# Optimization experiments

Measured on AMD Instinct MI355X. Metric: run time of the kernel, lower is better.

The kernel has to match this reference:

```python
import jax, jax.numpy as jnp
import numpy as np

B, S, D, H = 8, 1024, 1024, 16
DH = D // H
LN_EPS = 1e-5
SLOPE = 0.01  # nn.LeakyReLU default negative_slope


def _ln(x, g, b):
    m = x.mean(-1, keepdims=True)
    v = ((x - m) ** 2).mean(-1, keepdims=True)
    return (x - m) / jnp.sqrt(v + LN_EPS) * g + b


def _leaky(x):
    return jnp.where(x >= 0, x, SLOPE * x)


def setup_inputs() -> dict:
    key = jax.random.key(0)
    ks = jax.random.split(key, 6)
    q = jax.random.normal(ks[0], (B, S, D), dtype=jnp.float32)
    masks = jnp.ones((B, S), dtype=jnp.int32)  # all-valid mask (masked_fill is a no-op)
    w1 = jax.random.normal(ks[1], (D, D), dtype=jnp.float32) * 0.02
    b1 = jnp.zeros((D,), jnp.float32)
    w2 = jax.random.normal(ks[2], (D, D), dtype=jnp.float32) * 0.02
    b2 = jnp.zeros((D,), jnp.float32)
    ones = jnp.ones((D,), jnp.float32)
    zeros = jnp.zeros((D,), jnp.float32)
    return dict(q=q, masks=masks,
                w1=w1, b1=b1, ln1_g=ones, ln1_b=zeros,
                w2=w2, b2=b2, ln2_g=ones, ln2_b=zeros,
                anf_g=ones, anf_b=zeros,
                an1_g=ones, an1_b=zeros,
                an2_g=ones, an2_b=zeros)


def reference(q, masks, w1, b1, ln1_g, ln1_b, w2, b2, ln2_g, ln2_b,
              anf_g, anf_b, an1_g, an1_b, an2_g, an2_b):
    # --- multi-head cosine-similarity attention (k = v = q, no projections) ---
    qh = q.reshape(B, S, H, DH).transpose(0, 2, 1, 3)  # (B,H,S,DH) == separate_heads
    qn = qh / jnp.clip(jnp.linalg.norm(qh, axis=-1, keepdims=True), 1e-8)
    # cosine similarity scores, softmax over keys
    w = jax.nn.softmax(jnp.einsum('bhqd,bhkd->bhqk', qn, qn), axis=-1)
    # masked_fill AFTER softmax (faithful to source: mask per (batch, query))
    w = jnp.where(masks[:, None, :, None] == 0, jnp.float32(-1e9), w)
    heads = jnp.einsum('bhqk,bhkd->bhqd', w, qh)
    attn = heads.transpose(0, 2, 1, 3).reshape(B, S, D)  # concat_heads
    # --- add_norm1 (dropout=0.5 but eval mode => identity) ---
    y1 = _ln(q + attn, an1_g, an1_b)
    # --- PositionWiseFFN: Linear->LN->LeakyReLU x2, then internal AddNorm ---
    h = _leaky(_ln(y1 @ w1 + b1, ln1_g, ln1_b))
    y = _leaky(_ln(h @ w2 + b2, ln2_g, ln2_b))
    y2 = _ln(y1 + y, anf_g, anf_b)
    # --- add_norm2 ---
    return _ln(y1 + y2, an2_g, an2_b)
```

## Files before the change

### kernel.cpp

```cpp
#include <hip/hip_runtime.h>
#include <hip/hip_bf16.h>

#define BB 8
#define SS 1024
#define DD 1024
#define HH 16

typedef __attribute__((ext_vector_type(8))) short short8;
typedef __attribute__((ext_vector_type(8))) __bf16 bf16x8;
typedef __attribute__((ext_vector_type(4))) float f32x4;

__device__ inline float bf2f(unsigned short h){
  unsigned u = ((unsigned)h) << 16;
  return __builtin_bit_cast(float, u);
}
__device__ inline unsigned short f2bf(float f){
  unsigned u = __builtin_bit_cast(unsigned, f);
  u += 0x7fffu + ((u >> 16) & 1u);
  return (unsigned short)(u >> 16);
}
__device__ inline f32x4 mfma16(short8 a, short8 b, f32x4 c){
  return __builtin_amdgcn_mfma_f32_16x16x32_bf16(
      __builtin_bit_cast(bf16x8, a), __builtin_bit_cast(bf16x8, b), c, 0, 0, 0);
}

__global__ __launch_bounds__(256) void prep_w(const float* __restrict__ w1,
                                              const float* __restrict__ w2,
                                              unsigned short* __restrict__ w1T,
                                              unsigned short* __restrict__ w2T){
  __shared__ float tile[64][65];
  const float* src = blockIdx.z ? w2 : w1;
  unsigned short* dst = blockIdx.z ? w2T : w1T;
  int k0 = blockIdx.x * 64, n0 = blockIdx.y * 64;
  int tx = threadIdx.x & 63, ty = threadIdx.x >> 6;
#pragma unroll
  for (int r = 0; r < 16; ++r)
    tile[ty + 4*r][tx] = src[(k0 + ty + 4*r) * DD + n0 + tx];
  __syncthreads();
#pragma unroll
  for (int r = 0; r < 16; ++r)
    dst[(n0 + ty + 4*r) * DD + k0 + tx] = f2bf(tile[tx][ty + 4*r]);
}

__global__ __launch_bounds__(256) void prep_q(const float* __restrict__ q,
                                              unsigned short* __restrict__ kf,
                                              unsigned short* __restrict__ vf){
  __shared__ float tile[64][65];
  __shared__ float rinv[64];
  int bh = blockIdx.x >> 4, st = blockIdx.x & 15;
  int b = bh >> 4, h = bh & 15;
  int t = threadIdx.x;
  int tx = t & 63, ty = t >> 6;
  int srow = b * SS + st * 64;
#pragma unroll
  for (int r = 0; r < 16; ++r)
    tile[ty + 4*r][tx] = q[(size_t)(srow + ty + 4*r) * DD + h * 64 + tx];
  __syncthreads();
  {
    int s = t >> 2, p = t & 3;
    float ssum = 0.f;
#pragma unroll
    for (int i = 0; i < 16; ++i){ float v = tile[s][p*16 + i]; ssum += v * v; }
    ssum += __shfl_xor(ssum, 1);
    ssum += __shfl_xor(ssum, 2);
    if (p == 0) rinv[s] = 1.0f / fmaxf(sqrtf(ssum), 1e-8f);
  }
  __syncthreads();
#pragma unroll
  for (int v = 0; v < 2; ++v){
    int idx = t * 2 + v;
    int c_l = idx >> 6, lane = idx & 63;
    int hf = c_l & 1, ch = c_l >> 1;
    int s = ch * 16 + (lane & 15);
    int d0 = hf * 32 + (lane >> 4) * 8;
    float rv = rinv[s];
    short8 o;
#pragma unroll
    for (int e = 0; e < 8; ++e) o[e] = (short)f2bf(tile[s][d0 + e] * rv);
    *(short8*)(kf + ((size_t)(bh * 128 + st * 8 + c_l) * 64 + lane) * 8) = o;
  }
#pragma unroll
  for (int v = 0; v < 2; ++v){
    int idx = t * 2 + v;
    int kt2 = idx >> 8, db = (idx >> 6) & 3, lane = idx & 63;
    int d = db * 16 + (lane & 15);
    int k0 = kt2 * 32 + (lane >> 4) * 8;
    short8 o;
#pragma unroll
    for (int e = 0; e < 8; ++e) o[e] = (short)f2bf(tile[k0 + e][d]);
    *(short8*)(vf + ((size_t)((bh * 32 + st * 2 + kt2) * 4 + db) * 512 + lane * 8)) = o;
  }
}

__global__ __launch_bounds__(256, 4) void attn_kern(const unsigned short* __restrict__ kf,
                                                    const unsigned short* __restrict__ vf,
                                                    const int* __restrict__ masks,
                                                    unsigned short* __restrict__ attnb){
  __shared__ unsigned short Kb[2][4][64 * 8];
  __shared__ unsigned short Vb[2][4][64 * 8];
  __shared__ unsigned short Pw[4][32 * 40];
  __shared__ int anym;
  const int bh = blockIdx.x, b = bh >> 4, h = bh & 15;
  const int sq = blockIdx.y * 128;
  const int t = threadIdx.x, w = t >> 6, l = t & 63;
  const int lr = l & 15, lg = l >> 4;
  if (t == 0) anym = 0;
  __syncthreads();
  if (t < 128 && masks[b * SS + sq + t] == 0) anym = 1;

  short8 aQ[2][2];
#pragma unroll
  for (int m = 0; m < 2; ++m)
#pragma unroll
    for (int hf = 0; hf < 2; ++hf)
      aQ[m][hf] = *(const short8*)(kf +
          ((size_t)(bh * 128 + (blockIdx.y * 8 + w * 2 + m) * 2 + hf) * 64 + l) * 8);

  {
    const unsigned short* srcK = kf + ((size_t)(bh * 128 + 0 * 4 + w) * 64 + l) * 8;
    const unsigned short* srcV = vf + ((size_t)((bh * 32 + 0) * 4 + w) * 512 + l * 8);
    __builtin_amdgcn_global_load_lds((const __attribute__((address_space(1))) void*)srcK,
        (__attribute__((address_space(3))) void*)(&Kb[0][w][0]), 16, 0, 0);
    __builtin_amdgcn_global_load_lds((const __attribute__((address_space(1))) void*)srcV,
        (__attribute__((address_space(3))) void*)(&Vb[0][w][0]), 16, 0, 0);
  }
  __syncthreads();

  f32x4 o[2][4] = {};
  f32x4 rsum[2] = {{0.f,0.f,0.f,0.f},{0.f,0.f,0.f,0.f}};
  unsigned short* pw = &Pw[w][0];

  for (int it = 0; it < 32; ++it){
    const int cur = it & 1, nxt = cur ^ 1;
    if (it + 1 < 32){
      const unsigned short* srcK = kf + ((size_t)(bh * 128 + (it + 1) * 4 + w) * 64 + l) * 8;
      const unsigned short* srcV = vf + ((size_t)((bh * 32 + (it + 1)) * 4 + w) * 512 + l * 8);
      __builtin_amdgcn_global_load_lds((const __attribute__((address_space(1))) void*)srcK,
          (__attribute__((address_space(3))) void*)(&Kb[nxt][w][0]), 16, 0, 0);
      __builtin_amdgcn_global_load_lds((const __attribute__((address_space(1))) void*)srcV,
          (__attribute__((address_space(3))) void*)(&Vb[nxt][w][0]), 16, 0, 0);
    }
    short8 bK[2][2];
#pragma unroll
    for (int cc = 0; cc < 2; ++cc)
#pragma unroll
      for (int hf = 0; hf < 2; ++hf)
        bK[cc][hf] = *(const short8*)&Kb[cur][cc * 2 + hf][l * 8];
    f32x4 sc[2][2];
#pragma unroll
    for (int m = 0; m < 2; ++m)
#pragma unroll
      for (int cc = 0; cc < 2; ++cc){
        f32x4 z = {0.f, 0.f, 0.f, 0.f};
        z = mfma16(aQ[m][0], bK[cc][0], z);
        z = mfma16(aQ[m][1], bK[cc][1], z);
        sc[m][cc] = z;
      }
#pragma unroll
    for (int m = 0; m < 2; ++m)
#pragma unroll
      for (int cc = 0; cc < 2; ++cc)
#pragma unroll
        for (int j = 0; j < 4; ++j){
          float pv = __expf(sc[m][cc][j] - 1.0f);
          rsum[m][j] += pv;
          pw[(m * 16 + lg * 4 + j) * 40 + cc * 16 + lr] = f2bf(pv);
        }
    short8 aP[2];
#pragma unroll
    for (int m = 0; m < 2; ++m)
      aP[m] = *(const short8*)&pw[(m * 16 + lr) * 40 + lg * 8];
#pragma unroll
    for (int db = 0; db < 4; ++db){
      short8 bV = *(const short8*)&Vb[cur][db][l * 8];
      o[0][db] = mfma16(aP[0], bV, o[0][db]);
      o[1][db] = mfma16(aP[1], bV, o[1][db]);
    }
    __syncthreads();
  }

  f32x4 inv[2];
#pragma unroll
  for (int m = 0; m < 2; ++m)
#pragma unroll
    for (int j = 0; j < 4; ++j){
      float r = rsum[m][j];
      r += __shfl_xor(r, 1); r += __shfl_xor(r, 2);
      r += __shfl_xor(r, 4); r += __shfl_xor(r, 8);
      inv[m][j] = 1.0f / r;
    }
#pragma unroll
  for (int m = 0; m < 2; ++m)
#pragma unroll
    for (int db = 0; db < 4; ++db)
#pragma unroll
      for (int j = 0; j < 4; ++j){
        int row = sq + w * 32 + m * 16 + lg * 4 + j;
        float val = o[m][db][j] * inv[m][j];
        if (anym && masks[b * SS + row] == 0){
          int d_lr = lr;
          float vs = 0.f;
          for (int kt = 0; kt < 32; ++kt)
            for (int part = 0; part < 4; ++part){
              const unsigned short* vp = vf +
                  ((size_t)((bh * 32 + kt) * 4 + db) * 512 + (part * 16 + d_lr) * 8);
              for (int e = 0; e < 8; ++e) vs += bf2f(vp[e]);
            }
          val = -1e9f * vs;
        }
        attnb[(size_t)(b * SS + row) * DD + h * 64 + db * 16 + lr] = f2bf(val);
      }
}

__device__ inline float2 block_reduce2(float a, float bq){
  __shared__ float sm[8];
#pragma unroll
  for (int off = 1; off < 64; off <<= 1){
    a += __shfl_xor(a, off);
    bq += __shfl_xor(bq, off);
  }
  int w = threadIdx.x >> 6;
  if ((threadIdx.x & 63) == 0){ sm[2*w] = a; sm[2*w + 1] = bq; }
  __syncthreads();
  float2 r;
  r.x = sm[0] + sm[2] + sm[4] + sm[6];
  r.y = sm[1] + sm[3] + sm[5] + sm[7];
  __syncthreads();
  return r;
}

__global__ __launch_bounds__(256) void addnorm1(const float* __restrict__ q,
                                                const unsigned short* __restrict__ attnb,
                                                const float* __restrict__ g,
                                                const float* __restrict__ bt,
                                                float* __restrict__ y1f,
                                                unsigned short* __restrict__ y1b){
  int row = blockIdx.x, t = threadIdx.x;
  float4 qv = *(const float4*)(q + (size_t)row * DD + t * 4);
  ushort4 av = *(const ushort4*)(attnb + (size_t)row * DD + t * 4);
  float x[4] = { qv.x + bf2f(av.x), qv.y + bf2f(av.y), qv.z + bf2f(av.z), qv.w + bf2f(av.w) };
  float s = 0.f, ssq = 0.f;
#pragma unroll
  for (int i = 0; i < 4; ++i){ s += x[i]; ssq += x[i] * x[i]; }
  float2 r = block_reduce2(s, ssq);
  float m = r.x * (1.0f / DD);
  float rs = rsqrtf(r.y * (1.0f / DD) - m * m + 1e-5f);
  float4 gv = *(const float4*)(g + t * 4);
  float4 bv = *(const float4*)(bt + t * 4);
  float y[4] = { (x[0]-m)*rs*gv.x + bv.x, (x[1]-m)*rs*gv.y + bv.y,
                 (x[2]-m)*rs*gv.z + bv.z, (x[3]-m)*rs*gv.w + bv.w };
  *(float4*)(y1f + (size_t)row * DD + t * 4) = make_float4(y[0], y[1], y[2], y[3]);
  ushort4 ob = { f2bf(y[0]), f2bf(y[1]), f2bf(y[2]), f2bf(y[3]) };
  *(ushort4*)(y1b + (size_t)row * DD + t * 4) = ob;
}

__global__ __launch_bounds__(256, 2) void gemm_bias(const unsigned short* __restrict__ X,
                                                    const unsigned short* __restrict__ WT,
                                                    const float* __restrict__ bias,
                                                    unsigned short* __restrict__ out){
  __shared__ unsigned short As[128 * 32];
  __shared__ unsigned short Bs[128 * 32];
  int t = threadIdx.x, l = t & 63, w = t >> 6;
  int wm = w >> 1, wn = w & 1;
  int lr = l & 15, lg = l >> 4;
  int bm = blockIdx.x * 128, bn = blockIdx.y * 128;
  f32x4 acc[4][4] = {};
  int r = t >> 2, cb = (t & 3) * 8;
  for (int kt = 0; kt < 32; ++kt){
    __syncthreads();
    {
      const unsigned short* ga0 = X  + (size_t)(bm +      r) * 1024 + kt * 32 + cb;
      const unsigned short* ga1 = X  + (size_t)(bm + 64 + r) * 1024 + kt * 32 + cb;
      const unsigned short* gb0 = WT + (size_t)(bn +      r) * 1024 + kt * 32 + cb;
      const unsigned short* gb1 = WT + (size_t)(bn + 64 + r) * 1024 + kt * 32 + cb;
      __builtin_amdgcn_global_load_lds((const __attribute__((address_space(1))) void*)ga0,
          (__attribute__((address_space(3))) void*)((char*)As + w * 1024), 16, 0, 0);
      __builtin_amdgcn_global_load_lds((const __attribute__((address_space(1))) void*)ga1,
          (__attribute__((address_space(3))) void*)((char*)As + 4096 + w * 1024), 16, 0, 0);
      __builtin_amdgcn_global_load_lds((const __attribute__((address_space(1))) void*)gb0,
          (__attribute__((address_space(3))) void*)((char*)Bs + w * 1024), 16, 0, 0);
      __builtin_amdgcn_global_load_lds((const __attribute__((address_space(1))) void*)gb1,
          (__attribute__((address_space(3))) void*)((char*)Bs + 4096 + w * 1024), 16, 0, 0);
    }
    __syncthreads();
    short8 aA[4], bB[4];
#pragma unroll
    for (int i = 0; i < 4; ++i)
      aA[i] = *(const short8*)&As[(wm * 64 + i * 16 + lr) * 32 + lg * 8];
#pragma unroll
    for (int i = 0; i < 4; ++i)
      bB[i] = *(const short8*)&Bs[(wn * 64 + i * 16 + lr) * 32 + lg * 8];
#pragma unroll
    for (int mi = 0; mi < 4; ++mi)
#pragma unroll
      for (int ni = 0; ni < 4; ++ni)
        acc[mi][ni] = mfma16(aA[mi], bB[ni], acc[mi][ni]);
  }
#pragma unroll
  for (int ni = 0; ni < 4; ++ni){
    int col = bn + wn * 64 + ni * 16 + lr;
    float bv = bias[col];
#pragma unroll
    for (int mi = 0; mi < 4; ++mi){
      int row0 = bm + wm * 64 + mi * 16 + lg * 4;
#pragma unroll
      for (int j = 0; j < 4; ++j)
        out[(size_t)(row0 + j) * 1024 + col] = f2bf(acc[mi][ni][j] + bv);
    }
  }
}

__global__ __launch_bounds__(256) void ln_leaky(const unsigned short* __restrict__ in,
                                                const float* __restrict__ g,
                                                const float* __restrict__ bt,
                                                unsigned short* __restrict__ out){
  int row = blockIdx.x, t = threadIdx.x;
  ushort4 iv = *(const ushort4*)(in + (size_t)row * DD + t * 4);
  float x[4] = { bf2f(iv.x), bf2f(iv.y), bf2f(iv.z), bf2f(iv.w) };
  float s = 0.f, ssq = 0.f;
#pragma unroll
  for (int i = 0; i < 4; ++i){ s += x[i]; ssq += x[i] * x[i]; }
  float2 r = block_reduce2(s, ssq);
  float m = r.x * (1.0f / DD);
  float rs = rsqrtf(r.y * (1.0f / DD) - m * m + 1e-5f);
  float4 gv = *(const float4*)(g + t * 4);
  float4 bv = *(const float4*)(bt + t * 4);
  ushort4 ov;
  {
    float v0 = (x[0]-m)*rs*gv.x + bv.x; v0 = v0 >= 0.f ? v0 : 0.01f*v0; ov.x = f2bf(v0);
    float v1 = (x[1]-m)*rs*gv.y + bv.y; v1 = v1 >= 0.f ? v1 : 0.01f*v1; ov.y = f2bf(v1);
    float v2 = (x[2]-m)*rs*gv.z + bv.z; v2 = v2 >= 0.f ? v2 : 0.01f*v2; ov.z = f2bf(v2);
    float v3 = (x[3]-m)*rs*gv.w + bv.w; v3 = v3 >= 0.f ? v3 : 0.01f*v3; ov.w = f2bf(v3);
  }
  *(ushort4*)(out + (size_t)row * DD + t * 4) = ov;
}

__global__ __launch_bounds__(256) void final_kern(const unsigned short* __restrict__ g2,
                                                  const float* __restrict__ y1,
                                                  const float* __restrict__ ln2g, const float* __restrict__ ln2b,
                                                  const float* __restrict__ anfg, const float* __restrict__ anfb,
                                                  const float* __restrict__ an2g, const float* __restrict__ an2b,
                                                  float* __restrict__ out){
  int row = blockIdx.x, t = threadIdx.x;
  ushort4 iv = *(const ushort4*)(g2 + (size_t)row * DD + t * 4);
  float4 y1v = *(const float4*)(y1 + (size_t)row * DD + t * 4);
  float x[4] = { bf2f(iv.x), bf2f(iv.y), bf2f(iv.z), bf2f(iv.w) };
  float yy1[4] = { y1v.x, y1v.y, y1v.z, y1v.w };
  float s = 0.f, ssq = 0.f;
#pragma unroll
  for (int i = 0; i < 4; ++i){ s += x[i]; ssq += x[i]*x[i]; }
  float2 r = block_reduce2(s, ssq);
  float m = r.x * (1.0f / DD);
  float rs = rsqrtf(r.y * (1.0f / DD) - m*m + 1e-5f);
  float4 gv = *(const float4*)(ln2g + t * 4);
  float4 bv = *(const float4*)(ln2b + t * 4);
  float y[4] = { (x[0]-m)*rs*gv.x + bv.x, (x[1]-m)*rs*gv.y + bv.y,
                 (x[2]-m)*rs*gv.z + bv.z, (x[3]-m)*rs*gv.w + bv.w };
#pragma unroll
  for (int i = 0; i < 4; ++i) y[i] = y[i] >= 0.f ? y[i] : 0.01f*y[i];

  float tv[4]; s = 0.f; ssq = 0.f;
#pragma unroll
  for (int i = 0; i < 4; ++i){ tv[i] = yy1[i] + y[i]; s += tv[i]; ssq += tv[i]*tv[i]; }
  r = block_reduce2(s, ssq);
  m = r.x * (1.0f / DD);
  rs = rsqrtf(r.y * (1.0f / DD) - m*m + 1e-5f);
  gv = *(const float4*)(anfg + t * 4);
  bv = *(const float4*)(anfb + t * 4);
  float y2[4] = { (tv[0]-m)*rs*gv.x + bv.x, (tv[1]-m)*rs*gv.y + bv.y,
                  (tv[2]-m)*rs*gv.z + bv.z, (tv[3]-m)*rs*gv.w + bv.w };

  float u[4]; s = 0.f; ssq = 0.f;
#pragma unroll
  for (int i = 0; i < 4; ++i){ u[i] = yy1[i] + y2[i]; s += u[i]; ssq += u[i]*u[i]; }
  r = block_reduce2(s, ssq);
  m = r.x * (1.0f / DD);
  rs = rsqrtf(r.y * (1.0f / DD) - m*m + 1e-5f);
  gv = *(const float4*)(an2g + t * 4);
  bv = *(const float4*)(an2b + t * 4);
  float4 ov = { (u[0]-m)*rs*gv.x + bv.x, (u[1]-m)*rs*gv.y + bv.y,
                (u[2]-m)*rs*gv.z + bv.z, (u[3]-m)*rs*gv.w + bv.w };
  *(float4*)(out + (size_t)row * DD + t * 4) = ov;
}

extern "C" void kernel_launch(void* const* d_in, const int* in_sizes, int n_in,
                              void* d_out, int out_size, void* d_ws, size_t ws_size,
                              hipStream_t stream){
  const float* q    = (const float*)d_in[0];
  const int* masks  = (const int*)d_in[1];
  const float* w1   = (const float*)d_in[2];
  const float* b1   = (const float*)d_in[3];
  const float* ln1g = (const float*)d_in[4];
  const float* ln1b = (const float*)d_in[5];
  const float* w2   = (const float*)d_in[6];
  const float* b2   = (const float*)d_in[7];
  const float* ln2g = (const float*)d_in[8];
  const float* ln2b = (const float*)d_in[9];
  const float* anfg = (const float*)d_in[10];
  const float* anfb = (const float*)d_in[11];
  const float* an1g = (const float*)d_in[12];
  const float* an1b = (const float*)d_in[13];
  const float* an2g = (const float*)d_in[14];
  const float* an2b = (const float*)d_in[15];

  char* ws = (char*)d_ws;
  unsigned short* w1T  = (unsigned short*)(ws + 0);
  unsigned short* w2T  = (unsigned short*)(ws + 2097152);
  unsigned short* kf   = (unsigned short*)(ws + 4194304);
  unsigned short* vf   = (unsigned short*)(ws + 20971520);
  unsigned short* attn = (unsigned short*)(ws + 37748736);
  float*          y1f  = (float*)(ws + 54525952);
  unsigned short* y1b  = (unsigned short*)(ws + 88080384);
  unsigned short* g1   = kf;
  unsigned short* hbuf = vf;
  unsigned short* g2   = attn;
  float* outp = (float*)d_out;

  prep_w<<<dim3(16, 16, 2), 256, 0, stream>>>(w1, w2, w1T, w2T);
  prep_q<<<dim3(2048), 256, 0, stream>>>(q, kf, vf);
  attn_kern<<<dim3(128, 8), 256, 0, stream>>>(kf, vf, masks, attn);
  addnorm1<<<dim3(8192), 256, 0, stream>>>(q, attn, an1g, an1b, y1f, y1b);
  gemm_bias<<<dim3(64, 8), 256, 0, stream>>>(y1b, w1T, b1, g1);
  ln_leaky<<<dim3(8192), 256, 0, stream>>>(g1, ln1g, ln1b, hbuf);
  gemm_bias<<<dim3(64, 8), 256, 0, stream>>>(hbuf, w2T, b2, g2);
  final_kern<<<dim3(8192), 256, 0, stream>>>(g2, y1f, ln2g, ln2b, anfg, anfb, an2g, an2b, outp);
}
```

Measured before the change: 172.3 us.

## Split attention blocks into 8 waves and drop fp32 y1 buffer

The attention kernel now launches 512 threads with 8 waves, each handling 16 query rows instead of 32. K and V staging is split between waves 0-3 and 4-7, so each wave issues one async LDS load per iteration. This aims to raise occupancy and latency hiding while halving per-wave register state. Separately, the fp32 copy of y1 is no longer written: final_kern reads the bf16 y1 instead, which cuts memory traffic at the cost of residual precision.

New measurement: 167.0 us. -3.1%, faster.

```diff
diff --git a/kernel.cpp b/kernel.cpp
--- a/kernel.cpp
+++ b/kernel.cpp
@@ -92,13 +92,13 @@
   }
 }
 
-__global__ __launch_bounds__(256, 4) void attn_kern(const unsigned short* __restrict__ kf,
+__global__ __launch_bounds__(512, 8) void attn_kern(const unsigned short* __restrict__ kf,
                                                     const unsigned short* __restrict__ vf,
                                                     const int* __restrict__ masks,
                                                     unsigned short* __restrict__ attnb){
   __shared__ unsigned short Kb[2][4][64 * 8];
   __shared__ unsigned short Vb[2][4][64 * 8];
-  __shared__ unsigned short Pw[4][32 * 40];
+  __shared__ unsigned short Pw[8][16 * 40];
   __shared__ int anym;
   const int bh = blockIdx.x, b = bh >> 4, h = bh & 15;
   const int sq = blockIdx.y * 128;
@@ -108,37 +108,39 @@
   __syncthreads();
   if (t < 128 && masks[b * SS + sq + t] == 0) anym = 1;
 
-  short8 aQ[2][2];
-#pragma unroll
-  for (int m = 0; m < 2; ++m)
-#pragma unroll
-    for (int hf = 0; hf < 2; ++hf)
-      aQ[m][hf] = *(const short8*)(kf +
-          ((size_t)(bh * 128 + (blockIdx.y * 8 + w * 2 + m) * 2 + hf) * 64 + l) * 8);
-
-  {
-    const unsigned short* srcK = kf + ((size_t)(bh * 128 + 0 * 4 + w) * 64 + l) * 8;
-    const unsigned short* srcV = vf + ((size_t)((bh * 32 + 0) * 4 + w) * 512 + l * 8);
+  short8 aQ[2];
+#pragma unroll
+  for (int hf = 0; hf < 2; ++hf)
+    aQ[hf] = *(const short8*)(kf +
+        ((size_t)(bh * 128 + (blockIdx.y * 8 + w) * 2 + hf) * 64 + l) * 8);
+
+  if (w < 4){
+    const unsigned short* srcK = kf + ((size_t)(bh * 128 + w) * 64 + l) * 8;
     __builtin_amdgcn_global_load_lds((const __attribute__((address_space(1))) void*)srcK,
         (__attribute__((address_space(3))) void*)(&Kb[0][w][0]), 16, 0, 0);
+  } else {
+    const unsigned short* srcV = vf + ((size_t)((bh * 32 + 0) * 4 + (w - 4)) * 512 + l * 8);
     __builtin_amdgcn_global_load_lds((const __attribute__((address_space(1))) void*)srcV,
-        (__attribute__((address_space(3))) void*)(&Vb[0][w][0]), 16, 0, 0);
-  }
-  __syncthreads();
-
-  f32x4 o[2][4] = {};
-  f32x4 rsum[2] = {{0.f,0.f,0.f,0.f},{0.f,0.f,0.f,0.f}};
+        (__attribute__((address_space(3))) void*)(&Vb[0][w - 4][0]), 16, 0, 0);
+  }
+  __syncthreads();
+
+  f32x4 o[4] = {};
+  f32x4 rsum = {0.f, 0.f, 0.f, 0.f};
   unsigned short* pw = &Pw[w][0];
 
   for (int it = 0; it < 32; ++it){
     const int cur = it & 1, nxt = cur ^ 1;
     if (it + 1 < 32){
-      const unsigned short* srcK = kf + ((size_t)(bh * 128 + (it + 1) * 4 + w) * 64 + l) * 8;
-      const unsigned short* srcV = vf + ((size_t)((bh * 32 + (it + 1)) * 4 + w) * 512 + l * 8);
-      __builtin_amdgcn_global_load_lds((const __attribute__((address_space(1))) void*)srcK,
-          (__attribute__((address_space(3))) void*)(&Kb[nxt][w][0]), 16, 0, 0);
-      __builtin_amdgcn_global_load_lds((const __attribute__((address_space(1))) void*)srcV,
-          (__attribute__((address_space(3))) void*)(&Vb[nxt][w][0]), 16, 0, 0);
+      if (w < 4){
+        const unsigned short* srcK = kf + ((size_t)(bh * 128 + (it + 1) * 4 + w) * 64 + l) * 8;
+        __builtin_amdgcn_global_load_lds((const __attribute__((address_space(1))) void*)srcK,
+            (__attribute__((address_space(3))) void*)(&Kb[nxt][w][0]), 16, 0, 0);
+      } else {
+        const unsigned short* srcV = vf + ((size_t)((bh * 32 + (it + 1)) * 4 + (w - 4)) * 512 + l * 8);
+        __builtin_amdgcn_global_load_lds((const __attribute__((address_space(1))) void*)srcV,
+            (__attribute__((address_space(3))) void*)(&Vb[nxt][w - 4][0]), 16, 0, 0);
+      }
     }
     short8 bK[2][2];
 #pragma unroll
@@ -146,70 +148,57 @@
 #pragma unroll
       for (int hf = 0; hf < 2; ++hf)
         bK[cc][hf] = *(const short8*)&Kb[cur][cc * 2 + hf][l * 8];
-    f32x4 sc[2][2];
-#pragma unroll
-    for (int m = 0; m < 2; ++m)
-#pragma unroll
-      for (int cc = 0; cc < 2; ++cc){
-        f32x4 z = {0.f, 0.f, 0.f, 0.f};
-        z = mfma16(aQ[m][0], bK[cc][0], z);
-        z = mfma16(aQ[m][1], bK[cc][1], z);
-        sc[m][cc] = z;
+    f32x4 sc[2];
+#pragma unroll
+    for (int cc = 0; cc < 2; ++cc){
+      f32x4 z = {0.f, 0.f, 0.f, 0.f};
+      z = mfma16(aQ[0], bK[cc][0], z);
+      z = mfma16(aQ[1], bK[cc][1], z);
+      sc[cc] = z;
+    }
+#pragma unroll
+    for (int cc = 0; cc < 2; ++cc)
+#pragma unroll
+      for (int j = 0; j < 4; ++j){
+        float pv = __expf(sc[cc][j] - 1.0f);
+        rsum[j] += pv;
+        pw[(lg * 4 + j) * 40 + cc * 16 + lr] = f2bf(pv);
       }
-#pragma unroll
-    for (int m = 0; m < 2; ++m)
-#pragma unroll
-      for (int cc = 0; cc < 2; ++cc)
-#pragma unroll
-        for (int j = 0; j < 4; ++j){
-          float pv = __expf(sc[m][cc][j] - 1.0f);
-          rsum[m][j] += pv;
-          pw[(m * 16 + lg * 4 + j) * 40 + cc * 16 + lr] = f2bf(pv);
-        }
-    short8 aP[2];
-#pragma unroll
-    for (int m = 0; m < 2; ++m)
-      aP[m] = *(const short8*)&pw[(m * 16 + lr) * 40 + lg * 8];
+    short8 aP = *(const short8*)&pw[lr * 40 + lg * 8];
 #pragma unroll
     for (int db = 0; db < 4; ++db){
       short8 bV = *(const short8*)&Vb[cur][db][l * 8];
-      o[0][db] = mfma16(aP[0], bV, o[0][db]);
-      o[1][db] = mfma16(aP[1], bV, o[1][db]);
+      o[db] = mfma16(aP, bV, o[db]);
     }
     __syncthreads();
   }
 
-  f32x4 inv[2];
-#pragma unroll
-  for (int m = 0; m < 2; ++m)
+  f32x4 inv;
+#pragma unroll
+  for (int j = 0; j < 4; ++j){
+    float r = rsum[j];
+    r += __shfl_xor(r, 1); r += __shfl_xor(r, 2);
+    r += __shfl_xor(r, 4); r += __shfl_xor(r, 8);
+    inv[j] = 1.0f / r;
+  }
+#pragma unroll
+  for (int db = 0; db < 4; ++db)
 #pragma unroll
     for (int j = 0; j < 4; ++j){
-      float r = rsum[m][j];
-      r += __shfl_xor(r, 1); r += __shfl_xor(r, 2);
-      r += __shfl_xor(r, 4); r += __shfl_xor(r, 8);
-      inv[m][j] = 1.0f / r;
-    }
-#pragma unroll
-  for (int m = 0; m < 2; ++m)
-#pragma unroll
-    for (int db = 0; db < 4; ++db)
-#pragma unroll
-      for (int j = 0; j < 4; ++j){
-        int row = sq + w * 32 + m * 16 + lg * 4 + j;
-        float val = o[m][db][j] * inv[m][j];
-        if (anym && masks[b * SS + row] == 0){
-          int d_lr = lr;
-          float vs = 0.f;
-          for (int kt = 0; kt < 32; ++kt)
-            for (int part = 0; part < 4; ++part){
-              const unsigned short* vp = vf +
-                  ((size_t)((bh * 32 + kt) * 4 + db) * 512 + (part * 16 + d_lr) * 8);
-              for (int e = 0; e < 8; ++e) vs += bf2f(vp[e]);
-            }
-          val = -1e9f * vs;
-        }
-        attnb[(size_t)(b * SS + row) * DD + h * 64 + db * 16 + lr] = f2bf(val);
+      int row = sq + w * 16 + lg * 4 + j;
+      float val = o[db][j] * inv[j];
+      if (anym && masks[b * SS + row] == 0){
+        float vs = 0.f;
+        for (int kt = 0; kt < 32; ++kt)
+          for (int part = 0; part < 4; ++part){
+            const unsigned short* vp = vf +
+                ((size_t)((bh * 32 + kt) * 4 + db) * 512 + (part * 16 + lr) * 8);
+            for (int e = 0; e < 8; ++e) vs += bf2f(vp[e]);
+          }
+        val = -1e9f * vs;
       }
+      attnb[(size_t)(b * SS + row) * DD + h * 64 + db * 16 + lr] = f2bf(val);
+    }
 }
 
 __device__ inline float2 block_reduce2(float a, float bq){
@@ -233,7 +222,6 @@
                                                 const unsigned short* __restrict__ attnb,
                                                 const float* __restrict__ g,
                                                 const float* __restrict__ bt,
-                                                float* __restrict__ y1f,
                                                 unsigned short* __restrict__ y1b){
   int row = blockIdx.x, t = threadIdx.x;
   float4 qv = *(const float4*)(q + (size_t)row * DD + t * 4);
@@ -249,7 +237,6 @@
   float4 bv = *(const float4*)(bt + t * 4);
   float y[4] = { (x[0]-m)*rs*gv.x + bv.x, (x[1]-m)*rs*gv.y + bv.y,
                  (x[2]-m)*rs*gv.z + bv.z, (x[3]-m)*rs*gv.w + bv.w };
-  *(float4*)(y1f + (size_t)row * DD + t * 4) = make_float4(y[0], y[1], y[2], y[3]);
   ushort4 ob = { f2bf(y[0]), f2bf(y[1]), f2bf(y[2]), f2bf(y[3]) };
   *(ushort4*)(y1b + (size_t)row * DD + t * 4) = ob;
 }
@@ -336,16 +323,16 @@
 }
 
 __global__ __launch_bounds__(256) void final_kern(const unsigned short* __restrict__ g2,
-                                                  const float* __restrict__ y1,
+                                                  const unsigned short* __restrict__ y1,
                                                   const float* __restrict__ ln2g, const float* __restrict__ ln2b,
                                                   const float* __restrict__ anfg, const float* __restrict__ anfb,
                                                   const float* __restrict__ an2g, const float* __restrict__ an2b,
                                                   float* __restrict__ out){
   int row = blockIdx.x, t = threadIdx.x;
   ushort4 iv = *(const ushort4*)(g2 + (size_t)row * DD + t * 4);
-  float4 y1v = *(const float4*)(y1 + (size_t)row * DD + t * 4);
+  ushort4 y1v = *(const ushort4*)(y1 + (size_t)row * DD + t * 4);
   float x[4] = { bf2f(iv.x), bf2f(iv.y), bf2f(iv.z), bf2f(iv.w) };
-  float yy1[4] = { y1v.x, y1v.y, y1v.z, y1v.w };
+  float yy1[4] = { bf2f(y1v.x), bf2f(y1v.y), bf2f(y1v.z), bf2f(y1v.w) };
   float s = 0.f, ssq = 0.f;
 #pragma unroll
   for (int i = 0; i < 4; ++i){ s += x[i]; ssq += x[i]*x[i]; }
@@ -409,8 +396,7 @@
   unsigned short* kf   = (unsigned short*)(ws + 4194304);
   unsigned short* vf   = (unsigned short*)(ws + 20971520);
   unsigned short* attn = (unsigned short*)(ws + 37748736);
-  float*          y1f  = (float*)(ws + 54525952);
-  unsigned short* y1b  = (unsigned short*)(ws + 88080384);
+  unsigned short* y1b  = (unsigned short*)(ws + 54525952);
   unsigned short* g1   = kf;
   unsigned short* hbuf = vf;
   unsigned short* g2   = attn;
@@ -418,10 +404,10 @@
 
   prep_w<<<dim3(16, 16, 2), 256, 0, stream>>>(w1, w2, w1T, w2T);
   prep_q<<<dim3(2048), 256, 0, stream>>>(q, kf, vf);
-  attn_kern<<<dim3(128, 8), 256, 0, stream>>>(kf, vf, masks, attn);
-  addnorm1<<<dim3(8192), 256, 0, stream>>>(q, attn, an1g, an1b, y1f, y1b);
+  attn_kern<<<dim3(128, 8), 512, 0, stream>>>(kf, vf, masks, attn);
+  addnorm1<<<dim3(8192), 256, 0, stream>>>(q, attn, an1g, an1b, y1b);
   gemm_bias<<<dim3(64, 8), 256, 0, stream>>>(y1b, w1T, b1, g1);
   ln_leaky<<<dim3(8192), 256, 0, stream>>>(g1, ln1g, ln1b, hbuf);
   gemm_bias<<<dim3(64, 8), 256, 0, stream>>>(hbuf, w2T, b2, g2);
-  final_kern<<<dim3(8192), 256, 0, stream>>>(g2, y1f, ln2g, ln2b, anfg, anfb, an2g, an2b, outp);
-}
+  final_kern<<<dim3(8192), 256, 0, stream>>>(g2, y1b, ln2g, ln2b, anfg, anfb, an2g, an2b, outp);
+}
```
